# Kernel tuning notes

Measured on AMD Instinct MI355X. Metric: run time of the kernel, lower is better.

## Reference

```python
import jax, jax.numpy as jnp
import numpy as np

B, T, D, H, R, N = 16, 1024, 1024, 256, 64, 8


def setup_inputs() -> dict:
    key = jax.random.key(0)
    ks = jax.random.split(key, 8)
    s = lambda k, shape, fan: jax.random.normal(k, shape, jnp.float32) / np.sqrt(fan)
    return {
        "x": jax.random.normal(ks[0], (B, T, D), jnp.float32),
        "W_base": s(ks[1], (D, D), D),
        "b_base": jnp.zeros((D,), jnp.float32),
        "W_enc": s(ks[2], (N, D, H), D),
        "b_enc": jnp.zeros((N, H), jnp.float32),
        "W_dec": s(ks[3], (N, H, D), H),
        "b_dec": jnp.zeros((N, D), jnp.float32),
        "W_down": s(ks[4], (N, D, R), D),
        "b_down": jnp.zeros((N, R), jnp.float32),
        "W_up": s(ks[5], (N, R, D), R),
        "b_up": jnp.zeros((N, D), jnp.float32),
        "connected_idx": jnp.arange(N, dtype=jnp.int32),
    }


def reference(x, W_base, b_base, W_enc, b_enc, W_dec, b_dec,
              W_down, b_down, W_up, b_up, connected_idx):
    # Base layer: Linear(D, D)
    base = jnp.einsum("btd,de->bte", x, W_base) + b_base

    # All discriminators in parallel (stack_module_state + vmap equivalent).
    # Autoencoder reconstruction loss per (discriminator, sample).
    h = jax.nn.relu(jnp.einsum("btd,ndh->nbth", x, W_enc) + b_enc[:, None, None, :])
    recon = jnp.einsum("nbth,nhd->nbtd", h, W_dec) + b_dec[:, None, None, :]
    losses = jnp.mean((recon - x[None]) ** 2, axis=(2, 3))  # [N, B]

    # Per-sample routing: argmin over discriminators -> connected adapter id.
    top1 = jnp.argmin(losses, axis=0)          # [B]
    adp = connected_idx[top1]                  # [B]

    # Gather selected adapter params (stack_module_state of chosen adapters)
    # and apply per-sample (vmap + functional_call equivalent).
    Wd, bd = W_down[adp], b_down[adp]          # [B,D,R], [B,R]
    Wu, bu = W_up[adp], b_up[adp]              # [B,R,D], [B,D]
    mid = jax.nn.relu(jnp.einsum("btd,bdr->btr", x, Wd) + bd[:, None, :])
    adapter_out = jnp.einsum("btr,brd->btd", mid, Wu) + bu[:, None, :]

    return base + adapter_out
```

## Files before the change

kernel.cpp:

```cpp
#include <hip/hip_runtime.h>
#include <stdint.h>

#define B_  16
#define T_  1024
#define D_  1024
#define H_  256
#define R_  64
#define N_  8
#define BT_ (B_ * T_)

typedef unsigned short u16;
typedef __bf16 bf16_t;
typedef bf16_t bf16x8 __attribute__((ext_vector_type(8)));
typedef float f32x4 __attribute__((ext_vector_type(4)));

__device__ __forceinline__ u16 f2bf(float f) {
    union { float f; uint32_t u; } v; v.f = f;
    uint32_t u = v.u;
    u += 0x7FFFu + ((u >> 16) & 1u);
    return (u16)(u >> 16);
}


__global__ __launch_bounds__(256) void cvt_x_kernel(const float* __restrict__ in,
                                                    u16* __restrict__ outp, int n4) {
    int i = blockIdx.x * 256 + threadIdx.x;
    if (i >= n4) return;
    float4 v = reinterpret_cast<const float4*>(in)[i];
    ushort4 o;
    o.x = f2bf(v.x); o.y = f2bf(v.y); o.z = f2bf(v.z); o.w = f2bf(v.w);
    reinterpret_cast<ushort4*>(outp)[i] = o;
}

__global__ __launch_bounds__(256) void transpose_cvt_kernel(const float* __restrict__ in,
                                                            u16* __restrict__ outp,
                                                            int Rr, int Cc) {
    __shared__ u16 tile[64][65];
    const size_t zofs = (size_t)blockIdx.z * Rr * Cc;
    const float* src = in + zofs;
    u16* dst = outp + zofs;
    const int r0 = blockIdx.y * 64, c0 = blockIdx.x * 64;
    const int tx = threadIdx.x & 63, ty = threadIdx.x >> 6;
#pragma unroll
    for (int i = 0; i < 16; i++) {
        int r = i * 4 + ty;
        tile[r][tx] = f2bf(src[(size_t)(r0 + r) * Cc + (c0 + tx)]);
    }
    __syncthreads();
#pragma unroll
    for (int i = 0; i < 16; i++) {
        int r = i * 4 + ty;
        dst[(size_t)(c0 + r) * Rr + (r0 + tx)] = tile[tx][r];
    }
}

__global__ __launch_bounds__(256) void enc_loss_kernel(
    const u16* __restrict__ xb, const float* __restrict__ x,
    const u16* __restrict__ Wenc_t,
    const float* __restrict__ b_enc,
    const u16* __restrict__ Wdec_t,
    const float* __restrict__ b_dec,
    float* __restrict__ losses) {

    __shared__ u16 lds_a[64 * 32];
    __shared__ u16 lds_b[256 * 32];
    __shared__ u16 lds_h[64 * 264];
    __shared__ float red[256];

    const int n = blockIdx.y;
    const int r0 = blockIdx.x * 64;
    const int bsamp = r0 >> 10;
    const int t = threadIdx.x;
    const int w = t >> 6;
    const int l = t & 63;
    const int lr = l & 15;
    const int lq = l >> 4;
    const int lk = lq * 8;

    const u16* We = Wenc_t + (size_t)n * H_ * D_;
    const u16* Wd = Wdec_t + (size_t)n * D_ * H_;

    const f32x4 fzero = {0.f, 0.f, 0.f, 0.f};
    f32x4 acc[4][4];
#pragma unroll
    for (int mt = 0; mt < 4; mt++)
#pragma unroll
        for (int nt = 0; nt < 4; nt++) acc[mt][nt] = fzero;

    for (int ks = 0; ks < 32; ks++) {
        const int k0 = ks * 32;
        __syncthreads();
        {
            int row = t >> 2, kc = t & 3;
            *reinterpret_cast<uint4*>(&lds_a[row * 32 + kc * 8]) =
                *reinterpret_cast<const uint4*>(&xb[(size_t)(r0 + row) * D_ + k0 + kc * 8]);
        }
#pragma unroll
        for (int i = 0; i < 4; i++) {
            int ch = i * 256 + t;
            int row = ch >> 2, kc = ch & 3;
            *reinterpret_cast<uint4*>(&lds_b[row * 32 + kc * 8]) =
                *reinterpret_cast<const uint4*>(&We[(size_t)row * D_ + k0 + kc * 8]);
        }
        __syncthreads();
        bf16x8 af[4], bfr[4];
#pragma unroll
        for (int mt = 0; mt < 4; mt++)
            af[mt] = *reinterpret_cast<const bf16x8*>(&lds_a[(mt * 16 + lr) * 32 + lk]);
#pragma unroll
        for (int nt = 0; nt < 4; nt++)
            bfr[nt] = *reinterpret_cast<const bf16x8*>(&lds_b[(w * 64 + nt * 16 + lr) * 32 + lk]);
#pragma unroll
        for (int mt = 0; mt < 4; mt++)
#pragma unroll
            for (int nt = 0; nt < 4; nt++)
                acc[mt][nt] = __builtin_amdgcn_mfma_f32_16x16x32_bf16(af[mt], bfr[nt], acc[mt][nt], 0, 0, 0);
    }
    __syncthreads();
#pragma unroll
    for (int mt = 0; mt < 4; mt++)
#pragma unroll
        for (int nt = 0; nt < 4; nt++) {
            int hc = w * 64 + nt * 16 + lr;
            float bias = b_enc[n * H_ + hc];
#pragma unroll
            for (int r = 0; r < 4; r++) {
                int row = mt * 16 + lq * 4 + r;
                float v2 = acc[mt][nt][r] + bias;
                lds_h[row * 264 + hc] = f2bf(v2 > 0.f ? v2 : 0.f);
            }
        }
    __syncthreads();

    float lacc = 0.f;
    for (int chk = 0; chk < 4; chk++) {
#pragma unroll
        for (int mt = 0; mt < 4; mt++)
#pragma unroll
            for (int nt = 0; nt < 4; nt++) acc[mt][nt] = fzero;
        for (int ks = 0; ks < 8; ks++) {
            __syncthreads();
#pragma unroll
            for (int i = 0; i < 4; i++) {
                int c2 = i * 256 + t;
                int row = c2 >> 2, kc = c2 & 3;
                *reinterpret_cast<uint4*>(&lds_b[row * 32 + kc * 8]) =
                    *reinterpret_cast<const uint4*>(&Wd[(size_t)(chk * 256 + row) * H_ + ks * 32 + kc * 8]);
            }
            __syncthreads();
            bf16x8 af[4], bfr[4];
#pragma unroll
            for (int mt = 0; mt < 4; mt++)
                af[mt] = *reinterpret_cast<const bf16x8*>(&lds_h[(mt * 16 + lr) * 264 + ks * 32 + lk]);
#pragma unroll
            for (int nt = 0; nt < 4; nt++)
                bfr[nt] = *reinterpret_cast<const bf16x8*>(&lds_b[(w * 64 + nt * 16 + lr) * 32 + lk]);
#pragma unroll
            for (int mt = 0; mt < 4; mt++)
#pragma unroll
                for (int nt = 0; nt < 4; nt++)
                    acc[mt][nt] = __builtin_amdgcn_mfma_f32_16x16x32_bf16(af[mt], bfr[nt], acc[mt][nt], 0, 0, 0);
        }
#pragma unroll
        for (int mt = 0; mt < 4; mt++)
#pragma unroll
            for (int nt = 0; nt < 4; nt++) {
                int d = chk * 256 + w * 64 + nt * 16 + lr;
                float bias = b_dec[n * D_ + d];
#pragma unroll
                for (int r = 0; r < 4; r++) {
                    int row = mt * 16 + lq * 4 + r;
                    float recon = acc[mt][nt][r] + bias;
                    float diff = recon - x[(size_t)(r0 + row) * D_ + d];
                    lacc += diff * diff;
                }
            }
    }

    red[t] = lacc;
    __syncthreads();
    for (int s = 128; s > 0; s >>= 1) {
        if (t < s) red[t] += red[t + s];
        __syncthreads();
    }
    if (t == 0) atomicAdd(&losses[n * B_ + bsamp], red[0]);
}

__global__ void argmin_kernel(const float* __restrict__ losses,
                              const int* __restrict__ cidx,
                              int* __restrict__ adp) {
    int b = threadIdx.x;
    if (b < B_) {
        float best = losses[b];
        int bi = 0;
        for (int n = 1; n < N_; n++) {
            float v = losses[n * B_ + b];
            if (v < best) { best = v; bi = n; }
        }
        adp[b] = cidx[bi];
    }
}

__global__ __launch_bounds__(64) void down_kernel(
    const u16* __restrict__ xb,
    const u16* __restrict__ Wdown_t,
    const float* __restrict__ b_down,
    const int* __restrict__ adp,
    u16* __restrict__ mid) {
    __shared__ u16 lds_a[64 * 32];
    __shared__ u16 lds_b[64 * 32];
    const int r0 = blockIdx.x * 64;
    const int n = adp[r0 >> 10];
    const u16* Wd = Wdown_t + (size_t)n * R_ * D_;
    const int l = threadIdx.x;
    const int lr = l & 15, lq = l >> 4, lk = lq * 8;
    const f32x4 fzero = {0.f, 0.f, 0.f, 0.f};
    f32x4 acc[4][4];
#pragma unroll
    for (int mt = 0; mt < 4; mt++)
#pragma unroll
        for (int nt = 0; nt < 4; nt++) acc[mt][nt] = fzero;
    for (int ks = 0; ks < 32; ks++) {
        const int k0 = ks * 32;
        __syncthreads();
#pragma unroll
        for (int i = 0; i < 4; i++) {
            int ch = i * 64 + l;
            int row = ch >> 2, kc = ch & 3;
            *reinterpret_cast<uint4*>(&lds_a[row * 32 + kc * 8]) =
                *reinterpret_cast<const uint4*>(&xb[(size_t)(r0 + row) * D_ + k0 + kc * 8]);
            *reinterpret_cast<uint4*>(&lds_b[row * 32 + kc * 8]) =
                *reinterpret_cast<const uint4*>(&Wd[(size_t)row * D_ + k0 + kc * 8]);
        }
        __syncthreads();
        bf16x8 af[4], bfr[4];
#pragma unroll
        for (int mt = 0; mt < 4; mt++)
            af[mt] = *reinterpret_cast<const bf16x8*>(&lds_a[(mt * 16 + lr) * 32 + lk]);
#pragma unroll
        for (int nt = 0; nt < 4; nt++)
            bfr[nt] = *reinterpret_cast<const bf16x8*>(&lds_b[(nt * 16 + lr) * 32 + lk]);
#pragma unroll
        for (int mt = 0; mt < 4; mt++)
#pragma unroll
            for (int nt = 0; nt < 4; nt++)
                acc[mt][nt] = __builtin_amdgcn_mfma_f32_16x16x32_bf16(af[mt], bfr[nt], acc[mt][nt], 0, 0, 0);
    }
#pragma unroll
    for (int mt = 0; mt < 4; mt++)
#pragma unroll
        for (int nt = 0; nt < 4; nt++) {
            int col = nt * 16 + lr;
            float bias = b_down[n * R_ + col];
#pragma unroll
            for (int r = 0; r < 4; r++) {
                int row = mt * 16 + lq * 4 + r;
                float v2 = acc[mt][nt][r] + bias;
                mid[(size_t)(r0 + row) * R_ + col] = f2bf(v2 > 0.f ? v2 : 0.f);
            }
        }
}

__global__ __launch_bounds__(256) void out_kernel(
    const u16* __restrict__ xb,
    const u16* __restrict__ Wb_t,
    const float* __restrict__ b_base,
    const u16* __restrict__ mid,
    const u16* __restrict__ Wup_t,
    const float* __restrict__ b_up,
    const int* __restrict__ adp,
    float* __restrict__ outp) {
    __shared__ u16 lds_a[128 * 32];
    __shared__ u16 lds_b[128 * 32];
    const int c0 = blockIdx.x * 128;
    const int r0 = blockIdx.y * 128;
    const int n = adp[r0 >> 10];
    const int t = threadIdx.x, w = t >> 6, l = t & 63;
    const int wm = (w >> 1) * 64, wn = (w & 1) * 64;
    const int lr = l & 15, lq = l >> 4, lk = lq * 8;
    const f32x4 fzero = {0.f, 0.f, 0.f, 0.f};
    f32x4 acc[4][4];
#pragma unroll
    for (int mt = 0; mt < 4; mt++)
#pragma unroll
        for (int nt = 0; nt < 4; nt++) acc[mt][nt] = fzero;

    for (int ks = 0; ks < 32; ks++) {
        const int k0 = ks * 32;
        __syncthreads();
#pragma unroll
        for (int i = 0; i < 2; i++) {
            int ch = i * 256 + t;
            int row = ch >> 2, kc = ch & 3;
            *reinterpret_cast<uint4*>(&lds_a[row * 32 + kc * 8]) =
                *reinterpret_cast<const uint4*>(&xb[(size_t)(r0 + row) * D_ + k0 + kc * 8]);
            *reinterpret_cast<uint4*>(&lds_b[row * 32 + kc * 8]) =
                *reinterpret_cast<const uint4*>(&Wb_t[(size_t)(c0 + row) * D_ + k0 + kc * 8]);
        }
        __syncthreads();
        bf16x8 af[4], bfr[4];
#pragma unroll
        for (int mt = 0; mt < 4; mt++)
            af[mt] = *reinterpret_cast<const bf16x8*>(&lds_a[(wm + mt * 16 + lr) * 32 + lk]);
#pragma unroll
        for (int nt = 0; nt < 4; nt++)
            bfr[nt] = *reinterpret_cast<const bf16x8*>(&lds_b[(wn + nt * 16 + lr) * 32 + lk]);
#pragma unroll
        for (int mt = 0; mt < 4; mt++)
#pragma unroll
            for (int nt = 0; nt < 4; nt++)
                acc[mt][nt] = __builtin_amdgcn_mfma_f32_16x16x32_bf16(af[mt], bfr[nt], acc[mt][nt], 0, 0, 0);
    }

    const u16* Wu = Wup_t + (size_t)n * D_ * R_;
    for (int ks = 0; ks < 2; ks++) {
        const int k0 = ks * 32;
        __syncthreads();
#pragma unroll
        for (int i = 0; i < 2; i++) {
            int ch = i * 256 + t;
            int row = ch >> 2, kc = ch & 3;
            *reinterpret_cast<uint4*>(&lds_a[row * 32 + kc * 8]) =
                *reinterpret_cast<const uint4*>(&mid[(size_t)(r0 + row) * R_ + k0 + kc * 8]);
            *reinterpret_cast<uint4*>(&lds_b[row * 32 + kc * 8]) =
                *reinterpret_cast<const uint4*>(&Wu[(size_t)(c0 + row) * R_ + k0 + kc * 8]);
        }
        __syncthreads();
        bf16x8 af[4], bfr[4];
#pragma unroll
        for (int mt = 0; mt < 4; mt++)
            af[mt] = *reinterpret_cast<const bf16x8*>(&lds_a[(wm + mt * 16 + lr) * 32 + lk]);
#pragma unroll
        for (int nt = 0; nt < 4; nt++)
            bfr[nt] = *reinterpret_cast<const bf16x8*>(&lds_b[(wn + nt * 16 + lr) * 32 + lk]);
#pragma unroll
        for (int mt = 0; mt < 4; mt++)
#pragma unroll
            for (int nt = 0; nt < 4; nt++)
                acc[mt][nt] = __builtin_amdgcn_mfma_f32_16x16x32_bf16(af[mt], bfr[nt], acc[mt][nt], 0, 0, 0);
    }

#pragma unroll
    for (int mt = 0; mt < 4; mt++)
#pragma unroll
        for (int nt = 0; nt < 4; nt++) {
            int gc = c0 + wn + nt * 16 + lr;
            float bias = b_base[gc] + b_up[n * D_ + gc];
#pragma unroll
            for (int r = 0; r < 4; r++) {
                int row = r0 + wm + mt * 16 + lq * 4 + r;
                outp[(size_t)row * D_ + gc] = acc[mt][nt][r] + bias;
            }
        }
}

extern "C" void kernel_launch(void* const* d_in, const int* in_sizes, int n_in,
                              void* d_out, int out_size, void* d_ws, size_t ws_size,
                              hipStream_t stream) {
    const float* x      = (const float*)d_in[0];
    const float* W_base = (const float*)d_in[1];
    const float* b_base = (const float*)d_in[2];
    const float* W_enc  = (const float*)d_in[3];
    const float* b_enc  = (const float*)d_in[4];
    const float* W_dec  = (const float*)d_in[5];
    const float* b_dec  = (const float*)d_in[6];
    const float* W_down = (const float*)d_in[7];
    const float* b_down = (const float*)d_in[8];
    const float* W_up   = (const float*)d_in[9];
    const float* b_up   = (const float*)d_in[10];
    const int*   cidx   = (const int*)d_in[11];
    float* outp = (float*)d_out;
    (void)in_sizes; (void)n_in; (void)out_size; (void)ws_size;

    char* p = (char*)d_ws;
    u16* xb      = (u16*)p; p += (size_t)BT_ * D_ * 2;
    u16* Wb_t    = (u16*)p; p += (size_t)D_ * D_ * 2;
    u16* Wenc_t  = (u16*)p; p += (size_t)N_ * H_ * D_ * 2;
    u16* Wdec_t  = (u16*)p; p += (size_t)N_ * D_ * H_ * 2;
    u16* Wdown_t = (u16*)p; p += (size_t)N_ * R_ * D_ * 2;
    u16* Wup_t   = (u16*)p; p += (size_t)N_ * D_ * R_ * 2;
    u16* mid     = (u16*)p; p += (size_t)BT_ * R_ * 2;
    float* losses = (float*)p; p += 256;
    int* adp      = (int*)p; p += 256;

    hipMemsetAsync(losses, 0, N_ * B_ * sizeof(float), stream);

    cvt_x_kernel<<<(BT_ * D_ / 4 + 255) / 256, 256, 0, stream>>>(x, xb, BT_ * D_ / 4);
    transpose_cvt_kernel<<<dim3(D_ / 64, D_ / 64, 1),  256, 0, stream>>>(W_base, Wb_t,    D_, D_);
    transpose_cvt_kernel<<<dim3(H_ / 64, D_ / 64, N_), 256, 0, stream>>>(W_enc,  Wenc_t,  D_, H_);
    transpose_cvt_kernel<<<dim3(D_ / 64, H_ / 64, N_), 256, 0, stream>>>(W_dec,  Wdec_t,  H_, D_);
    transpose_cvt_kernel<<<dim3(R_ / 64, D_ / 64, N_), 256, 0, stream>>>(W_down, Wdown_t, D_, R_);
    transpose_cvt_kernel<<<dim3(D_ / 64, R_ / 64, N_), 256, 0, stream>>>(W_up,   Wup_t,   R_, D_);

    enc_loss_kernel<<<dim3(BT_ / 64, N_), 256, 0, stream>>>(xb, x, Wenc_t, b_enc, Wdec_t, b_dec, losses);
    argmin_kernel<<<1, 64, 0, stream>>>(losses, cidx, adp);
    down_kernel<<<BT_ / 64, 64, 0, stream>>>(xb, Wdown_t, b_down, adp, mid);
    out_kernel<<<dim3(D_ / 128, BT_ / 128), 256, 0, stream>>>(xb, Wb_t, b_base, mid, Wup_t, b_up, adp, outp);
}
```

Measured before the change: 488.9 us.

## Use direct global-to-LDS loads and split-K down projection across four waves

Global-to-register-to-LDS tile copies in the encoder/loss, down and output GEMMs are replaced with global_load_lds 16-byte direct loads, so staging no longer passes through VGPRs. The down kernel goes from one wave to four waves per block. Each wave handles a quarter of the K dimension in its own LDS region, and the partial sums are reduced through 64KB of shared memory before the bias and ReLU. The gains are fewer instructions and registers per load and more parallelism in the under-occupied down kernel. The costs are the larger LDS footprint, an extra reduction pass, and reliance on the lane-linear LDS layout that global_load_lds writes.

After: 456.7 us. -6.6%, faster.

```diff
diff --git a/kernel.cpp b/kernel.cpp
--- a/kernel.cpp
+++ b/kernel.cpp
@@ -19,6 +19,12 @@
     uint32_t u = v.u;
     u += 0x7FFFu + ((u >> 16) & 1u);
     return (u16)(u >> 16);
+}
+
+__device__ __forceinline__ void gl_lds16(const void* g, void* l) {
+    __builtin_amdgcn_global_load_lds(
+        (const __attribute__((address_space(1))) void*)g,
+        (__attribute__((address_space(3))) void*)l, 16, 0, 0);
 }
 
 
@@ -91,16 +97,16 @@
         const int k0 = ks * 32;
         __syncthreads();
         {
-            int row = t >> 2, kc = t & 3;
-            *reinterpret_cast<uint4*>(&lds_a[row * 32 + kc * 8]) =
-                *reinterpret_cast<const uint4*>(&xb[(size_t)(r0 + row) * D_ + k0 + kc * 8]);
+            int c = w * 64 + l, row = c >> 2, kc = c & 3;
+            gl_lds16(&xb[(size_t)(r0 + row) * D_ + k0 + kc * 8],
+                     (char*)lds_a + w * 1024);
         }
 #pragma unroll
         for (int i = 0; i < 4; i++) {
-            int ch = i * 256 + t;
-            int row = ch >> 2, kc = ch & 3;
-            *reinterpret_cast<uint4*>(&lds_b[row * 32 + kc * 8]) =
-                *reinterpret_cast<const uint4*>(&We[(size_t)row * D_ + k0 + kc * 8]);
+            int j = w * 4 + i;
+            int c = j * 64 + l, row = c >> 2, kc = c & 3;
+            gl_lds16(&We[(size_t)row * D_ + k0 + kc * 8],
+                     (char*)lds_b + j * 1024);
         }
         __syncthreads();
         bf16x8 af[4], bfr[4];
@@ -142,10 +148,10 @@
             __syncthreads();
 #pragma unroll
             for (int i = 0; i < 4; i++) {
-                int c2 = i * 256 + t;
-                int row = c2 >> 2, kc = c2 & 3;
-                *reinterpret_cast<uint4*>(&lds_b[row * 32 + kc * 8]) =
-                    *reinterpret_cast<const uint4*>(&Wd[(size_t)(chk * 256 + row) * H_ + ks * 32 + kc * 8]);
+                int j = w * 4 + i;
+                int c = j * 64 + l, row = c >> 2, kc = c & 3;
+                gl_lds16(&Wd[(size_t)(chk * 256 + row) * H_ + ks * 32 + kc * 8],
+                         (char*)lds_b + j * 1024);
             }
             __syncthreads();
             bf16x8 af[4], bfr[4];
@@ -201,64 +207,70 @@
     }
 }
 
-__global__ __launch_bounds__(64) void down_kernel(
+__global__ __launch_bounds__(256) void down_kernel(
     const u16* __restrict__ xb,
     const u16* __restrict__ Wdown_t,
     const float* __restrict__ b_down,
     const int* __restrict__ adp,
     u16* __restrict__ mid) {
-    __shared__ u16 lds_a[64 * 32];
-    __shared__ u16 lds_b[64 * 32];
+    __shared__ char smem[65536];
     const int r0 = blockIdx.x * 64;
     const int n = adp[r0 >> 10];
     const u16* Wd = Wdown_t + (size_t)n * R_ * D_;
-    const int l = threadIdx.x;
+    const int t = threadIdx.x, w = t >> 6, l = t & 63;
     const int lr = l & 15, lq = l >> 4, lk = lq * 8;
+    char* wbase = smem + w * 8192;
+    const u16* sa = (const u16*)wbase;
+    const u16* sb = (const u16*)(wbase + 4096);
     const f32x4 fzero = {0.f, 0.f, 0.f, 0.f};
     f32x4 acc[4][4];
 #pragma unroll
     for (int mt = 0; mt < 4; mt++)
 #pragma unroll
         for (int nt = 0; nt < 4; nt++) acc[mt][nt] = fzero;
-    for (int ks = 0; ks < 32; ks++) {
-        const int k0 = ks * 32;
+
+    for (int ks2 = 0; ks2 < 8; ks2++) {
+        const int k0 = (w * 8 + ks2) * 32;
         __syncthreads();
 #pragma unroll
         for (int i = 0; i < 4; i++) {
-            int ch = i * 64 + l;
-            int row = ch >> 2, kc = ch & 3;
-            *reinterpret_cast<uint4*>(&lds_a[row * 32 + kc * 8]) =
-                *reinterpret_cast<const uint4*>(&xb[(size_t)(r0 + row) * D_ + k0 + kc * 8]);
-            *reinterpret_cast<uint4*>(&lds_b[row * 32 + kc * 8]) =
-                *reinterpret_cast<const uint4*>(&Wd[(size_t)row * D_ + k0 + kc * 8]);
+            int c = i * 64 + l, row = c >> 2, kc = c & 3;
+            gl_lds16(&xb[(size_t)(r0 + row) * D_ + k0 + kc * 8], wbase + i * 1024);
+            gl_lds16(&Wd[(size_t)row * D_ + k0 + kc * 8], wbase + 4096 + i * 1024);
         }
         __syncthreads();
         bf16x8 af[4], bfr[4];
 #pragma unroll
         for (int mt = 0; mt < 4; mt++)
-            af[mt] = *reinterpret_cast<const bf16x8*>(&lds_a[(mt * 16 + lr) * 32 + lk]);
+            af[mt] = *reinterpret_cast<const bf16x8*>(&sa[(mt * 16 + lr) * 32 + lk]);
 #pragma unroll
         for (int nt = 0; nt < 4; nt++)
-            bfr[nt] = *reinterpret_cast<const bf16x8*>(&lds_b[(nt * 16 + lr) * 32 + lk]);
+            bfr[nt] = *reinterpret_cast<const bf16x8*>(&sb[(nt * 16 + lr) * 32 + lk]);
 #pragma unroll
         for (int mt = 0; mt < 4; mt++)
 #pragma unroll
             for (int nt = 0; nt < 4; nt++)
                 acc[mt][nt] = __builtin_amdgcn_mfma_f32_16x16x32_bf16(af[mt], bfr[nt], acc[mt][nt], 0, 0, 0);
     }
-#pragma unroll
-    for (int mt = 0; mt < 4; mt++)
-#pragma unroll
-        for (int nt = 0; nt < 4; nt++) {
-            int col = nt * 16 + lr;
-            float bias = b_down[n * R_ + col];
-#pragma unroll
-            for (int r = 0; r < 4; r++) {
-                int row = mt * 16 + lq * 4 + r;
-                float v2 = acc[mt][nt][r] + bias;
-                mid[(size_t)(r0 + row) * R_ + col] = f2bf(v2 > 0.f ? v2 : 0.f);
-            }
-        }
+
+    __syncthreads();
+    float* pr = (float*)smem;
+#pragma unroll
+    for (int mt = 0; mt < 4; mt++)
+#pragma unroll
+        for (int nt = 0; nt < 4; nt++)
+#pragma unroll
+            for (int r = 0; r < 4; r++)
+                pr[w * 4096 + (mt * 16 + lq * 4 + r) * 64 + nt * 16 + lr] = acc[mt][nt][r];
+    __syncthreads();
+#pragma unroll
+    for (int ei = 0; ei < 16; ei++) {
+        int e = ei * 256 + t;
+        float s = pr[e] + pr[4096 + e] + pr[8192 + e] + pr[12288 + e];
+        int row = e >> 6, col = e & 63;
+        float v = s + b_down[n * R_ + col];
+        mid[(size_t)(r0 + row) * R_ + col] = f2bf(v > 0.f ? v : 0.f);
+    }
 }
 
 __global__ __launch_bounds__(256) void out_kernel(
@@ -290,12 +302,12 @@
         __syncthreads();
 #pragma unroll
         for (int i = 0; i < 2; i++) {
-            int ch = i * 256 + t;
-            int row = ch >> 2, kc = ch & 3;
-            *reinterpret_cast<uint4*>(&lds_a[row * 32 + kc * 8]) =
-                *reinterpret_cast<const uint4*>(&xb[(size_t)(r0 + row) * D_ + k0 + kc * 8]);
-            *reinterpret_cast<uint4*>(&lds_b[row * 32 + kc * 8]) =
-                *reinterpret_cast<const uint4*>(&Wb_t[(size_t)(c0 + row) * D_ + k0 + kc * 8]);
+            int j = w * 2 + i;
+            int c = j * 64 + l, row = c >> 2, kc = c & 3;
+            gl_lds16(&xb[(size_t)(r0 + row) * D_ + k0 + kc * 8],
+                     (char*)lds_a + j * 1024);
+            gl_lds16(&Wb_t[(size_t)(c0 + row) * D_ + k0 + kc * 8],
+                     (char*)lds_b + j * 1024);
         }
         __syncthreads();
         bf16x8 af[4], bfr[4];
@@ -318,12 +330,12 @@
         __syncthreads();
 #pragma unroll
         for (int i = 0; i < 2; i++) {
-            int ch = i * 256 + t;
-            int row = ch >> 2, kc = ch & 3;
-            *reinterpret_cast<uint4*>(&lds_a[row * 32 + kc * 8]) =
-                *reinterpret_cast<const uint4*>(&mid[(size_t)(r0 + row) * R_ + k0 + kc * 8]);
-            *reinterpret_cast<uint4*>(&lds_b[row * 32 + kc * 8]) =
-                *reinterpret_cast<const uint4*>(&Wu[(size_t)(c0 + row) * R_ + k0 + kc * 8]);
+            int j = w * 2 + i;
+            int c = j * 64 + l, row = c >> 2, kc = c & 3;
+            gl_lds16(&mid[(size_t)(r0 + row) * R_ + k0 + kc * 8],
+                     (char*)lds_a + j * 1024);
+            gl_lds16(&Wu[(size_t)(c0 + row) * R_ + k0 + kc * 8],
+                     (char*)lds_b + j * 1024);
         }
         __syncthreads();
         bf16x8 af[4], bfr[4];
@@ -394,6 +406,6 @@
 
     enc_loss_kernel<<<dim3(BT_ / 64, N_), 256, 0, stream>>>(xb, x, Wenc_t, b_enc, Wdec_t, b_dec, losses);
     argmin_kernel<<<1, 64, 0, stream>>>(losses, cidx, adp);
-    down_kernel<<<BT_ / 64, 64, 0, stream>>>(xb, Wdown_t, b_down, adp, mid);
+    down_kernel<<<BT_ / 64, 256, 0, stream>>>(xb, Wdown_t, b_down, adp, mid);
     out_kernel<<<dim3(D_ / 128, BT_ / 128), 256, 0, stream>>>(xb, Wb_t, b_base, mid, Wup_t, b_up, adp, outp);
 }
```
